# Kernel optimization log

Measured on AMD Instinct MI355X. Metric: run time of the kernel, lower is better.

Reference implementation:

```python
import jax, jax.numpy as jnp
import numpy as np

EPS = 1e-3  # Keras LayerNormalization default epsilon


def layernorm(x, g, b):
    mu = jnp.mean(x, axis=-1, keepdims=True)
    var = jnp.var(x, axis=-1, keepdims=True)
    return (x - mu) * jax.lax.rsqrt(var + EPS) * g + b


def setup_inputs() -> dict:
    key = jax.random.key(0)
    ks = jax.random.split(key, 16)
    B, T, C = 2, 2048, 1024
    F = 4 * C
    std = 0.02
    inp = {
        "x": jax.random.normal(ks[0], (B, T, C), jnp.float32),
        "ln1_g": jnp.ones((C,), jnp.float32),
        "ln1_b": jnp.zeros((C,), jnp.float32),
        "Wq": std * jax.random.normal(ks[1], (C, C), jnp.float32),
        "bq": jnp.zeros((C,), jnp.float32),
        "Wk": std * jax.random.normal(ks[2], (C, C), jnp.float32),
        "bk": jnp.zeros((C,), jnp.float32),
        "Wv": std * jax.random.normal(ks[3], (C, C), jnp.float32),
        "bv": jnp.zeros((C,), jnp.float32),
        "ln2_g": jnp.ones((C,), jnp.float32),
        "ln2_b": jnp.zeros((C,), jnp.float32),
        "W1": std * jax.random.normal(ks[4], (C, F), jnp.float32),
        "b1": jnp.zeros((F,), jnp.float32),
        "W2": std * jax.random.normal(ks[5], (F, C), jnp.float32),
        "b2": jnp.zeros((C,), jnp.float32),
    }
    return inp


N_HEADS = 16


def reference(x, ln1_g, ln1_b, Wq, bq, Wk, bk, Wv, bv, ln2_g, ln2_b, W1, b1, W2, b2):
    B, T, C = x.shape
    H = N_HEADS
    D = C // H

    h = layernorm(x, ln1_g, ln1_b)
    # [B,T,C] -> [B,H,T,D]
    def split_heads(y):
        return y.reshape(B, T, H, D).transpose(0, 2, 1, 3)

    q = split_heads(h @ Wq + bq)
    k = split_heads(h @ Wk + bk)
    v = split_heads(h @ Wv + bv)

    # Faithful to original: scores = K @ Q^T, i.e. scores[i,j] = k_i . q_j
    scores = jnp.einsum("bhid,bhjd->bhij", k, q) / jnp.sqrt(jnp.float32(D))
    causal = jnp.tril(jnp.ones((T, T), bool))  # [T,T]
    scores = jnp.where(causal[None, None], scores, -jnp.inf)
    w = jax.nn.softmax(scores, axis=-1)
    attn = jnp.einsum("bhij,bhjd->bhid", w, v)  # [B,H,T,D]
    attn = attn.transpose(0, 2, 1, 3).reshape(B, T, C)
    x = x + attn

    h2 = layernorm(x, ln2_g, ln2_b)
    ffn = jax.nn.gelu(h2 @ W1 + b1, approximate=False) @ W2 + b2
    x = x + ffn
    return x
```

## Files before the change

kernel.cpp:

```cpp
#include <hip/hip_runtime.h>
#include <hip/hip_bf16.h>
#include <math.h>

typedef __hip_bfloat16 bf16;
typedef __attribute__((ext_vector_type(8))) short bf16x8;
typedef __attribute__((ext_vector_type(4))) float f32x4;

__device__ __forceinline__ unsigned short f2bf_rne(float f) {
  unsigned u = __float_as_uint(f);
  u += 0x7fffu + ((u >> 16) & 1u);
  return (unsigned short)(u >> 16);
}
__device__ __forceinline__ float bf2f(unsigned short s) {
  return __uint_as_float(((unsigned)s) << 16);
}

__device__ __forceinline__ float gelu_fast(float v) {
  float u = v * (0.7978845608f + 0.0356774081f * v * v);
  float t = __builtin_amdgcn_exp2f(u * 2.8853900818f);
  float r = __builtin_amdgcn_rcpf(t + 1.0f);
  return v - v * r;
}

#define GLOBAL_AS __attribute__((address_space(1)))
#define LDS_AS __attribute__((address_space(3)))
__device__ __forceinline__ void gl2lds16(const void* g, void* l) {
  __builtin_amdgcn_global_load_lds((const GLOBAL_AS void*)g, (LDS_AS void*)l, 16, 0, 0);
}

__device__ __forceinline__ int swz8(int f, int nwg) {
  return (f & 7) * (nwg >> 3) + (f >> 3);
}

__device__ __forceinline__ void ln_body(const float* __restrict__ x,
                                        const float* __restrict__ g,
                                        const float* __restrict__ b,
                                        bf16* __restrict__ h, int row, int t) {
  const float4 xv = ((const float4*)(x + (size_t)row * 1024))[t];
  float s = xv.x + xv.y + xv.z + xv.w;
  float sq = xv.x * xv.x + xv.y * xv.y + xv.z * xv.z + xv.w * xv.w;
  #pragma unroll
  for (int m = 1; m < 64; m <<= 1) { s += __shfl_xor(s, m); sq += __shfl_xor(sq, m); }
  __shared__ float ps[4], pq[4];
  if ((t & 63) == 0) { ps[t >> 6] = s; pq[t >> 6] = sq; }
  __syncthreads();
  s = ps[0] + ps[1] + ps[2] + ps[3];
  sq = pq[0] + pq[1] + pq[2] + pq[3];
  float mean = s * (1.0f / 1024.0f);
  float var = sq * (1.0f / 1024.0f) - mean * mean;
  float rs = rsqrtf(var + 1e-3f);
  float4 gv = ((const float4*)g)[t];
  float4 bv = ((const float4*)b)[t];
  ushort4 o;
  o.x = f2bf_rne((xv.x - mean) * rs * gv.x + bv.x);
  o.y = f2bf_rne((xv.y - mean) * rs * gv.y + bv.y);
  o.z = f2bf_rne((xv.z - mean) * rs * gv.z + bv.z);
  o.w = f2bf_rne((xv.w - mean) * rs * gv.w + bv.w);
  ((ushort4*)(h + (size_t)row * 1024))[t] = o;
}

__global__ __launch_bounds__(256) void ln_kernel(const float* __restrict__ x,
                                                 const float* __restrict__ g,
                                                 const float* __restrict__ b,
                                                 bf16* __restrict__ h) {
  ln_body(x, g, b, h, blockIdx.x, threadIdx.x);
}

__device__ __forceinline__ void tr_tile(const float* __restrict__ W, bf16* __restrict__ WT,
                                        int R, int Cc, int bx, int by, int t) {
  __shared__ float tile[32][33];
  int tx = t & 31, ty = t >> 5;
  #pragma unroll
  for (int k = 0; k < 4; k++) {
    int rr = ty + k * 8;
    tile[rr][tx] = W[(size_t)(by + rr) * Cc + bx + tx];
  }
  __syncthreads();
  unsigned short* out = reinterpret_cast<unsigned short*>(WT);
  #pragma unroll
  for (int k = 0; k < 4; k++) {
    int rr = ty + k * 8;
    out[(size_t)(bx + rr) * R + by + tx] = f2bf_rne(tile[tx][rr]);
  }
}

__global__ __launch_bounds__(256) void prep_fused(const float* __restrict__ x,
                                                  const float* __restrict__ ln1g,
                                                  const float* __restrict__ ln1b,
                                                  bf16* __restrict__ h,
                                                  const float* __restrict__ Wq,
                                                  const float* __restrict__ Wk,
                                                  const float* __restrict__ Wv,
                                                  const float* __restrict__ W1,
                                                  const float* __restrict__ W2,
                                                  bf16* __restrict__ WqkT,
                                                  bf16* __restrict__ W1T,
                                                  bf16* __restrict__ W2T) {
  int id = blockIdx.x, t = threadIdx.x;
  if (id < 4096) { ln_body(x, ln1g, ln1b, h, id, t); return; }
  id -= 4096;
  if (id < 3072) {
    int sect = id >> 10, r = id & 1023;
    const float* W = sect == 0 ? Wq : (sect == 1 ? Wk : Wv);
    bf16* WT = WqkT + (size_t)sect * 1048576;
    tr_tile(W, WT, 1024, 1024, (r & 31) * 32, (r >> 5) * 32, t);
  } else if (id < 7168) {
    int r = id - 3072;
    tr_tile(W1, W1T, 1024, 4096, (r & 127) * 32, (r >> 7) * 32, t);
  } else {
    int r = id - 7168;
    tr_tile(W2, W2T, 4096, 1024, (r & 31) * 32, (r >> 5) * 32, t);
  }
}

__device__ __forceinline__ void mainloop_256(const bf16* __restrict__ A,
                                             const bf16* __restrict__ BT,
                                             int lda, int nk, int m0, int n0,
                                             char* ldsb, int t,
                                             f32x4 (&acc)[8][4]) {
  const int lane = t & 63, wave = t >> 6;
  const int l = lane & 15, quad = lane >> 4;
  const int wm = (wave >> 2) * 128, wn = (wave & 3) * 64;
  const int srow = wave * 8 + (lane >> 3);
  const int scol = ((lane & 7) ^ (lane >> 3)) * 8;
  const int grp0 = (quad ^ (l & 7)) * 16;
  const int grp1 = ((4 + quad) ^ (l & 7)) * 16;

  bf16x8 a[4][2], b01[2][2], b23[2][2];

  auto stA = [&](int buf, int half, int kt) {
    const bf16* s = A + (size_t)(m0 + half * 128 + srow) * lda + kt * 64 + scol;
    char* d = ldsb + buf * 65536 + half * 16384 + wave * 1024;
    gl2lds16(s, d);
    gl2lds16(s + (size_t)64 * lda, d + 8192);
  };
  auto stB = [&](int buf, int half, int kt) {
    const bf16* s = BT + (size_t)(n0 + half * 128 + srow) * lda + kt * 64 + scol;
    char* d = ldsb + buf * 65536 + 32768 + half * 16384 + wave * 1024;
    gl2lds16(s, d);
    gl2lds16(s + (size_t)64 * lda, d + 8192);
  };
  auto rdA = [&](int buf, int mh) {
    const char* base = ldsb + buf * 65536 + (wm + mh * 64 + l) * 128;
    #pragma unroll
    for (int ii = 0; ii < 4; ii++) {
      a[ii][0] = *(const bf16x8*)(base + ii * 2048 + grp0);
      a[ii][1] = *(const bf16x8*)(base + ii * 2048 + grp1);
    }
  };
  auto rdB = [&](int buf, int nh, bf16x8 (&bb)[2][2]) {
    const char* base = ldsb + buf * 65536 + 32768 + (wn + nh * 32 + l) * 128;
    #pragma unroll
    for (int jj = 0; jj < 2; jj++) {
      bb[jj][0] = *(const bf16x8*)(base + jj * 2048 + grp0);
      bb[jj][1] = *(const bf16x8*)(base + jj * 2048 + grp1);
    }
  };
  auto mm4 = [&](int mi, bf16x8 (&bb)[2][2], int nj) {
    #pragma unroll
    for (int ii = 0; ii < 4; ii++)
      #pragma unroll
      for (int jj = 0; jj < 2; jj++) {
        acc[mi + ii][nj + jj] = __builtin_amdgcn_mfma_f32_16x16x32_bf16(
            a[ii][0], bb[jj][0], acc[mi + ii][nj + jj], 0, 0, 0);
        acc[mi + ii][nj + jj] = __builtin_amdgcn_mfma_f32_16x16x32_bf16(
            a[ii][1], bb[jj][1], acc[mi + ii][nj + jj], 0, 0, 0);
      }
  };

#define BARX() __builtin_amdgcn_s_barrier()
#define LGKM0() do { asm volatile("s_waitcnt lgkmcnt(0)" ::: "memory"); \
                     __builtin_amdgcn_sched_barrier(0); } while (0)
#define HALF4(BC, DOA, SAB, SAK, DOB, SBB, SBK, VMN)                      \
  do {                                                                    \
    rdA(BC, 0); rdB(BC, 0, b01);                                          \
    if (DOA) stA(SAB, 0, SAK);                                            \
    BARX(); LGKM0();                                                      \
    __builtin_amdgcn_s_setprio(1); mm4(0, b01, 0);                        \
    __builtin_amdgcn_s_setprio(0); BARX();                                \
    rdB(BC, 1, b23);                                                      \
    if (DOA) stA(SAB, 1, SAK);                                            \
    BARX(); LGKM0();                                                      \
    __builtin_amdgcn_s_setprio(1); mm4(0, b23, 2);                        \
    __builtin_amdgcn_s_setprio(0); BARX();                                \
    rdA(BC, 1);                                                           \
    if (DOB) stB(SBB, 0, SBK);                                            \
    BARX(); LGKM0();                                                      \
    __builtin_amdgcn_s_setprio(1); mm4(4, b01, 0);                        \
    __builtin_amdgcn_s_setprio(0); BARX();                                \
    if (DOB) stB(SBB, 1, SBK);                                            \
    BARX();                                                               \
    __builtin_amdgcn_s_setprio(1); mm4(4, b23, 2);                        \
    __builtin_amdgcn_s_setprio(0);                                        \
    asm volatile("s_waitcnt vmcnt(" VMN ")" ::: "memory");                \
    BARX();                                                               \
  } while (0)

  const int nt = nk >> 6;
  stA(0, 0, 0); stA(0, 1, 0);
  stB(0, 0, 0); stB(0, 1, 0);
  stB(1, 0, 1); stB(1, 1, 1);
  asm volatile("s_waitcnt vmcnt(4)" ::: "memory");
  BARX();
  int tt = 0;
  for (; tt + 2 < nt; tt += 2) {
    HALF4(0, 1, 1, tt + 1, 1, 0, tt + 2, "4");
    HALF4(1, 1, 0, tt + 2, 1, 1, tt + 3, "4");
  }
  HALF4(0, 1, 1, tt + 1, 0, 0, 0, "0");
  HALF4(1, 0, 0, 0, 0, 0, 0, "0");
#undef HALF4
#undef LGKM0
#undef BARX
}

__global__ __launch_bounds__(512, 2) void gemm_ffn1(const bf16* __restrict__ A,
                                                    const bf16* __restrict__ BT,
                                                    const float* __restrict__ bias,
                                                    bf16* __restrict__ out,
                                                    int N, int K) {
  extern __shared__ char lds[];
  int t = threadIdx.x;
  int nf = swz8(blockIdx.x, gridDim.x);
  int n0 = (nf & 15) * 256, m0 = (nf >> 4) * 256;
  f32x4 acc[8][4];
  #pragma unroll
  for (int i = 0; i < 8; i++)
    #pragma unroll
    for (int j = 0; j < 4; j++) acc[i][j] = (f32x4){0.f, 0.f, 0.f, 0.f};
  mainloop_256(A, BT, K, K, m0, n0, lds, t, acc);

  int lane = t & 63, wave = t >> 6;
  int l = lane & 15, quad = lane >> 4;
  int wm = (wave >> 2) * 128, wn = (wave & 3) * 64;
  int r4 = quad * 4;
  unsigned short* os = reinterpret_cast<unsigned short*>(out);
  #pragma unroll
  for (int i = 0; i < 8; i++)
    #pragma unroll
    for (int j = 0; j < 4; j++) {
      int col = n0 + wn + j * 16 + l;
      float bval = bias[col];
      #pragma unroll
      for (int r = 0; r < 4; r++) {
        int row = m0 + wm + i * 16 + r4 + r;
        os[(size_t)row * N + col] = f2bf_rne(gelu_fast(acc[i][j][r] + bval));
      }
    }
}

__global__ __launch_bounds__(512, 2) void gemm_ffn2(const bf16* __restrict__ A,
                                                    const bf16* __restrict__ BT,
                                                    unsigned short* __restrict__ p0,
                                                    unsigned short* __restrict__ p1,
                                                    unsigned short* __restrict__ p2,
                                                    unsigned short* __restrict__ p3) {
  extern __shared__ char lds[];
  int t = threadIdx.x;
  int nf = swz8(blockIdx.x, gridDim.x);
  int n0 = (nf & 3) * 256, m0 = ((nf >> 2) & 15) * 256;
  int z = nf >> 6;
  f32x4 acc[8][4];
  #pragma unroll
  for (int i = 0; i < 8; i++)
    #pragma unroll
    for (int j = 0; j < 4; j++) acc[i][j] = (f32x4){0.f, 0.f, 0.f, 0.f};
  mainloop_256(A + z * 1024, BT + z * 1024, 4096, 1024, m0, n0, lds, t, acc);

  unsigned short* p = z == 0 ? p0 : (z == 1 ? p1 : (z == 2 ? p2 : p3));
  int lane = t & 63, wave = t >> 6;
  int l = lane & 15, quad = lane >> 4;
  int wm = (wave >> 2) * 128, wn = (wave & 3) * 64;
  int r4 = quad * 4;
  #pragma unroll
  for (int i = 0; i < 8; i++)
    #pragma unroll
    for (int j = 0; j < 4; j++) {
      int col = n0 + wn + j * 16 + l;
      #pragma unroll
      for (int r = 0; r < 4; r++) {
        int row = m0 + wm + i * 16 + r4 + r;
        p[(size_t)row * 1024 + col] = f2bf_rne(acc[i][j][r]);
      }
    }
}

__global__ __launch_bounds__(256) void reduce_ffn2(const unsigned short* __restrict__ p0,
                                                   const unsigned short* __restrict__ p1,
                                                   const unsigned short* __restrict__ p2,
                                                   const unsigned short* __restrict__ p3,
                                                   const float* __restrict__ x1,
                                                   const float* __restrict__ bias,
                                                   float* __restrict__ out) {
  int row = blockIdx.x, t = threadIdx.x;
  size_t base = (size_t)row * 1024;
  ushort4 a = ((const ushort4*)(p0 + base))[t];
  ushort4 b = ((const ushort4*)(p1 + base))[t];
  ushort4 c = ((const ushort4*)(p2 + base))[t];
  ushort4 d = ((const ushort4*)(p3 + base))[t];
  float4 xv = ((const float4*)(x1 + base))[t];
  float4 bv = ((const float4*)bias)[t];
  float4 o;
  o.x = (bf2f(a.x) + bf2f(b.x)) + (bf2f(c.x) + bf2f(d.x)) + xv.x + bv.x;
  o.y = (bf2f(a.y) + bf2f(b.y)) + (bf2f(c.y) + bf2f(d.y)) + xv.y + bv.y;
  o.z = (bf2f(a.z) + bf2f(b.z)) + (bf2f(c.z) + bf2f(d.z)) + xv.z + bv.z;
  o.w = (bf2f(a.w) + bf2f(b.w)) + (bf2f(c.w) + bf2f(d.w)) + xv.w + bv.w;
  ((float4*)(out + base))[t] = o;
}

__global__ __launch_bounds__(512, 2) void gemm_qkv(const bf16* __restrict__ A,
                                                   const bf16* __restrict__ BT,
                                                   const float* __restrict__ bq,
                                                   const float* __restrict__ bk,
                                                   const float* __restrict__ bv,
                                                   bf16* __restrict__ qb,
                                                   bf16* __restrict__ kb,
                                                   bf16* __restrict__ vt,
                                                   int K) {
  extern __shared__ char lds[];
  int t = threadIdx.x;
  int nf = swz8(blockIdx.x, gridDim.x);
  int n0 = (nf % 12) * 256, m0 = (nf / 12) * 256;
  f32x4 acc[8][4];
  #pragma unroll
  for (int i = 0; i < 8; i++)
    #pragma unroll
    for (int j = 0; j < 4; j++) acc[i][j] = (f32x4){0.f, 0.f, 0.f, 0.f};
  mainloop_256(A, BT, K, K, m0, n0, lds, t, acc);

  int lane = t & 63, wave = t >> 6;
  int l = lane & 15, quad = lane >> 4;
  int wm = (wave >> 2) * 128, wn = (wave & 3) * 64;
  int sect = n0 >> 10;
  const float* bias = sect == 0 ? bq : (sect == 1 ? bk : bv);
  int r4 = quad * 4;
  #pragma unroll
  for (int i = 0; i < 8; i++)
    #pragma unroll
    for (int j = 0; j < 4; j++) {
      int col = n0 + wn + j * 16 + l;
      int c1 = col & 1023;
      float bval = bias[c1];
      int row0 = m0 + wm + i * 16 + r4;
      if (sect < 2) {
        bf16* o = sect == 0 ? qb : kb;
        unsigned short* os = reinterpret_cast<unsigned short*>(o);
        #pragma unroll
        for (int r = 0; r < 4; r++)
          os[(size_t)(row0 + r) * 1024 + c1] = f2bf_rne(acc[i][j][r] + bval);
      } else {
        int hh = c1 >> 6, d = c1 & 63;
        int b = row0 >> 11, t0 = row0 & 2047;
        ushort4 pk;
        pk.x = f2bf_rne(acc[i][j][0] + bval);
        pk.y = f2bf_rne(acc[i][j][1] + bval);
        pk.z = f2bf_rne(acc[i][j][2] + bval);
        pk.w = f2bf_rne(acc[i][j][3] + bval);
        *(ushort4*)((unsigned short*)vt + (size_t)((b * 16 + hh) * 64 + d) * 2048 + t0) = pk;
      }
    }
}

__global__ __launch_bounds__(512, 4) void attn_mfma(const bf16* __restrict__ qb,
                                                    const bf16* __restrict__ kb,
                                                    const bf16* __restrict__ vt,
                                                    const float* __restrict__ x,
                                                    float* __restrict__ x1) {
  extern __shared__ char alds[];
  char* KVb = alds;
  char* Pb  = alds + 65536;
  int t = threadIdx.x;
  int bh = blockIdx.x;
  int b = bh >> 4, h = bh & 15;
  size_t qk_base = (size_t)b * 2048 * 1024 + (size_t)h * 64;
  size_t vt_base = (size_t)bh * 64 * 2048;
  int lane = t & 63, wave = t >> 6;
  int g = wave >> 2, w4 = wave & 3;
  int l = lane & 15, quad = lane >> 4;
  int sw = l & 7;
  int srow8 = lane >> 3;
  int scol = ((lane & 7) ^ srow8) * 8;
  const float cs = 0.125f * 1.44269504088896f;
  int it = 31 - blockIdx.y;
  int i0 = it * 64;
  int njt = it + 1;
  int iblk = i0 + w4 * 16;

  if (g == 0) {
    #pragma unroll
    for (int c = 0; c < 2; c++) {
      int rr = w4 * 16 + c * 8 + srow8;
      gl2lds16(kb + qk_base + (size_t)(i0 + rr) * 1024 + scol,
               Pb + w4 * 2048 + c * 1024);
      gl2lds16(qb + qk_base + (size_t)rr * 1024 + scol,
               KVb + w4 * 2048 + c * 1024);
      gl2lds16(vt + vt_base + (size_t)rr * 2048 + scol,
               KVb + 8192 + w4 * 2048 + c * 1024);
    }
  } else if (njt > 1) {
    #pragma unroll
    for (int c = 0; c < 2; c++) {
      int rr = w4 * 16 + c * 8 + srow8;
      gl2lds16(qb + qk_base + (size_t)(64 + rr) * 1024 + scol,
               KVb + 32768 + w4 * 2048 + c * 1024);
      gl2lds16(vt + vt_base + (size_t)rr * 2048 + 64 + scol,
               KVb + 32768 + 8192 + w4 * 2048 + c * 1024);
    }
  }
  __syncthreads();

  const char* qr = Pb + w4 * 2048 + l * 128;
  bf16x8 qf0 = *(const bf16x8*)(qr + ((quad ^ sw) * 16));
  bf16x8 qf1 = *(const bf16x8*)(qr + (((4 + quad) ^ sw) * 16));
  __syncthreads();

  float lsum = 0.f;
  f32x4 Oacc[4];
  #pragma unroll
  for (int dt = 0; dt < 4; dt++) Oacc[dt] = (f32x4){0.f, 0.f, 0.f, 0.f};

  char* Pw = Pb + wave * 2048 + l * 128;
  char* KVg = KVb + g * 32768;
  int nstep = (njt + 1) >> 1;
  int buf = 0;
  for (int s = 0; s < nstep; s++) {
    int jt = 2 * s + g;
    if (jt + 2 < njt) {
      int j1 = (jt + 2) * 64;
      #pragma unroll
      for (int c = 0; c < 2; c++) {
        int rr = w4 * 16 + c * 8 + srow8;
        gl2lds16(qb + qk_base + (size_t)(j1 + rr) * 1024 + scol,
                 KVg + (buf ^ 1) * 16384 + w4 * 2048 + c * 1024);
        gl2lds16(vt + vt_base + (size_t)rr * 2048 + j1 + scol,
                 KVg + (buf ^ 1) * 16384 + 8192 + w4 * 2048 + c * 1024);
      }
    }
    if (jt < njt) {
      int j0v = jt * 64;
      const bf16* Kb = (const bf16*)(KVg + buf * 16384);
      #pragma unroll
      for (int nt = 0; nt < 4; nt++) {
        int jb = j0v + nt * 16;
        uint2 pk;
        if (jb > iblk + 15) {
          pk.x = 0u; pk.y = 0u;
        } else {
          const bf16* kr = Kb + (nt * 16 + l) * 64;
          bf16x8 kf0 = *(const bf16x8*)(kr + ((quad ^ sw) * 8));
          bf16x8 kf1 = *(const bf16x8*)(kr + (((4 + quad) ^ sw) * 8));
          f32x4 sv = (f32x4){0.f, 0.f, 0.f, 0.f};
          __builtin_amdgcn_s_setprio(1);
          sv = __builtin_amdgcn_mfma_f32_16x16x32_bf16(kf0, qf0, sv, 0, 0, 0);
          sv = __builtin_amdgcn_mfma_f32_16x16x32_bf16(kf1, qf1, sv, 0, 0, 0);
          __builtin_amdgcn_s_setprio(0);
          float p0, p1, p2, p3;
          if (jb + 15 <= iblk) {
            p0 = __builtin_amdgcn_exp2f(sv[0] * cs);
            p1 = __builtin_amdgcn_exp2f(sv[1] * cs);
            p2 = __builtin_amdgcn_exp2f(sv[2] * cs);
            p3 = __builtin_amdgcn_exp2f(sv[3] * cs);
          } else {
            int i_ = iblk + l, jbase = jb + quad * 4;
            p0 = (jbase + 0 > i_) ? 0.f : __builtin_amdgcn_exp2f(sv[0] * cs);
            p1 = (jbase + 1 > i_) ? 0.f : __builtin_amdgcn_exp2f(sv[1] * cs);
            p2 = (jbase + 2 > i_) ? 0.f : __builtin_amdgcn_exp2f(sv[2] * cs);
            p3 = (jbase + 3 > i_) ? 0.f : __builtin_amdgcn_exp2f(sv[3] * cs);
          }
          lsum += (p0 + p1) + (p2 + p3);
          union { __hip_bfloat162 h2; unsigned u; } c0u, c1u;
          c0u.h2 = __float22bfloat162_rn(make_float2(p0, p1));
          c1u.h2 = __float22bfloat162_rn(make_float2(p2, p3));
          pk.x = c0u.u; pk.y = c1u.u;
        }
        *(uint2*)(Pw + (((nt * 2 + (quad >> 1)) ^ sw) << 4) + ((quad & 1) << 3)) = pk;
      }
      asm volatile("s_waitcnt lgkmcnt(0)" ::: "memory");

      bf16x8 ap0 = *(const bf16x8*)(Pw + ((quad ^ sw) << 4));
      bf16x8 ap1 = *(const bf16x8*)(Pw + (((4 + quad) ^ sw) << 4));
      const bf16* Vb = (const bf16*)(KVg + buf * 16384 + 8192);
      __builtin_amdgcn_s_setprio(1);
      #pragma unroll
      for (int dt = 0; dt < 4; dt++) {
        const bf16* vr = Vb + (dt * 16 + l) * 64;
        bf16x8 bv0 = *(const bf16x8*)(vr + ((quad ^ sw) * 8));
        bf16x8 bv1 = *(const bf16x8*)(vr + (((4 + quad) ^ sw) * 8));
        Oacc[dt] = __builtin_amdgcn_mfma_f32_16x16x32_bf16(ap0, bv0, Oacc[dt], 0, 0, 0);
        Oacc[dt] = __builtin_amdgcn_mfma_f32_16x16x32_bf16(ap1, bv1, Oacc[dt], 0, 0, 0);
      }
      __builtin_amdgcn_s_setprio(0);
    }
    __syncthreads();
    buf ^= 1;
  }

  float* F = (float*)KVb;
  int fbase = w4 * 1088;
  if (g == 1) {
    #pragma unroll
    for (int dt = 0; dt < 4; dt++)
      #pragma unroll
      for (int r = 0; r < 4; r++)
        F[fbase + (dt * 4 + r) * 64 + lane] = Oacc[dt][r];
    F[fbase + 1024 + lane] = lsum;
  }
  __syncthreads();
  if (g == 0) {
    #pragma unroll
    for (int dt = 0; dt < 4; dt++)
      #pragma unroll
      for (int r = 0; r < 4; r++)
        Oacc[dt][r] += F[fbase + (dt * 4 + r) * 64 + lane];
    lsum += F[fbase + 1024 + lane];
    lsum += __shfl_xor(lsum, 16);
    lsum += __shfl_xor(lsum, 32);
    #pragma unroll
    for (int r = 0; r < 4; r++) {
      float lv = __shfl(lsum, quad * 4 + r);
      float inv = 1.0f / lv;
      int row = iblk + quad * 4 + r;
      size_t gi = qk_base + (size_t)row * 1024;
      #pragma unroll
      for (int dt = 0; dt < 4; dt++) {
        int d = dt * 16 + l;
        x1[gi + d] = x[gi + d] + Oacc[dt][r] * inv;
      }
    }
  }
}

extern "C" void kernel_launch(void* const* d_in, const int* in_sizes, int n_in,
                              void* d_out, int out_size, void* d_ws, size_t ws_size,
                              hipStream_t stream) {
  const float* x    = (const float*)d_in[0];
  const float* ln1g = (const float*)d_in[1];
  const float* ln1b = (const float*)d_in[2];
  const float* Wq   = (const float*)d_in[3];
  const float* bq   = (const float*)d_in[4];
  const float* Wk   = (const float*)d_in[5];
  const float* bk   = (const float*)d_in[6];
  const float* Wv   = (const float*)d_in[7];
  const float* bv   = (const float*)d_in[8];
  const float* ln2g = (const float*)d_in[9];
  const float* ln2b = (const float*)d_in[10];
  const float* W1   = (const float*)d_in[11];
  const float* b1   = (const float*)d_in[12];
  const float* W2   = (const float*)d_in[13];
  const float* b2   = (const float*)d_in[14];

  char* ws = (char*)d_ws;
  float* x1  = (float*)(ws + 0);
  bf16* h    = (bf16*)(ws + 16777216);
  bf16* WqkT = (bf16*)(ws + 25165824);
  bf16* W1T  = (bf16*)(ws + 31457280);
  bf16* W2T  = (bf16*)(ws + 39845888);
  bf16* qb   = (bf16*)(ws + 48234496);
  bf16* kb   = (bf16*)(ws + 56623104);
  bf16* vt   = (bf16*)(ws + 65011712);
  bf16* act  = (bf16*)(ws + 73400320);

  static bool s_attr_done = false;
  if (!s_attr_done) {
    hipFuncSetAttribute(reinterpret_cast<const void*>(gemm_qkv),
                        hipFuncAttributeMaxDynamicSharedMemorySize, 131072);
    hipFuncSetAttribute(reinterpret_cast<const void*>(gemm_ffn1),
                        hipFuncAttributeMaxDynamicSharedMemorySize, 131072);
    hipFuncSetAttribute(reinterpret_cast<const void*>(gemm_ffn2),
                        hipFuncAttributeMaxDynamicSharedMemorySize, 131072);
    hipFuncSetAttribute(reinterpret_cast<const void*>(attn_mfma),
                        hipFuncAttributeMaxDynamicSharedMemorySize, 81920);
    s_attr_done = true;
  }

  prep_fused<<<15360, 256, 0, stream>>>(x, ln1g, ln1b, h,
                                        Wq, Wk, Wv, W1, W2, WqkT, W1T, W2T);
  gemm_qkv<<<192, 512, 131072, stream>>>(h, WqkT, bq, bk, bv, qb, kb, vt, 1024);
  attn_mfma<<<dim3(32, 32), 512, 81920, stream>>>(qb, kb, vt, x, x1);
  ln_kernel<<<4096, 256, 0, stream>>>(x1, ln2g, ln2b, h);
  gemm_ffn1<<<256, 512, 131072, stream>>>(h, W1T, b1, act, 4096, 1024);
  gemm_ffn2<<<256, 512, 131072, stream>>>(act, W2T,
      (unsigned short*)qb, (unsigned short*)kb, (unsigned short*)vt, (unsigned short*)h);
  reduce_ffn2<<<4096, 256, 0, stream>>>((const unsigned short*)qb, (const unsigned short*)kb,
                                        (const unsigned short*)vt, (const unsigned short*)h,
                                        x1, b2, (float*)d_out);
}
```

Baseline: 291.6 us.

## Fuse LN2 into attention and split-K reduce into FFN2 via atomic counters

Removes the standalone LayerNorm-2 kernel: the last attention block to finish for each row group, detected with an atomic counter, computes LN2 for those rows. Removes the standalone split-K reduction by having FFN2 blocks spin-wait on a per-tile counter until all four K-slices are written, then each block reduces a quarter of the tile. Also drops the s_setprio hints in the attention MFMA loops. This saves two launches and some memory traffic, but adds spin-waiting that can deadlock if the co-dependent blocks are not co-resident, and it serializes the LN2 work onto a few blocks.

```diff
diff --git a/kernel.cpp b/kernel.cpp
--- a/kernel.cpp
+++ b/kernel.cpp
@@ -59,13 +59,6 @@
   ((ushort4*)(h + (size_t)row * 1024))[t] = o;
 }
 
-__global__ __launch_bounds__(256) void ln_kernel(const float* __restrict__ x,
-                                                 const float* __restrict__ g,
-                                                 const float* __restrict__ b,
-                                                 bf16* __restrict__ h) {
-  ln_body(x, g, b, h, blockIdx.x, threadIdx.x);
-}
-
 __device__ __forceinline__ void tr_tile(const float* __restrict__ W, bf16* __restrict__ WT,
                                         int R, int Cc, int bx, int by, int t) {
   __shared__ float tile[32][33];
@@ -95,8 +88,10 @@
                                                   const float* __restrict__ W2,
                                                   bf16* __restrict__ WqkT,
                                                   bf16* __restrict__ W1T,
-                                                  bf16* __restrict__ W2T) {
+                                                  bf16* __restrict__ W2T,
+                                                  int* __restrict__ cnt) {
   int id = blockIdx.x, t = threadIdx.x;
+  if (id == 0 && t < 128) cnt[t] = 0;
   if (id < 4096) { ln_body(x, ln1g, ln1b, h, id, t); return; }
   id -= 4096;
   if (id < 3072) {
@@ -254,12 +249,17 @@
                                                     unsigned short* __restrict__ p0,
                                                     unsigned short* __restrict__ p1,
                                                     unsigned short* __restrict__ p2,
-                                                    unsigned short* __restrict__ p3) {
+                                                    unsigned short* __restrict__ p3,
+                                                    const float* __restrict__ x1,
+                                                    const float* __restrict__ bias,
+                                                    float* __restrict__ out,
+                                                    int* __restrict__ cnt) {
   extern __shared__ char lds[];
   int t = threadIdx.x;
   int nf = swz8(blockIdx.x, gridDim.x);
   int n0 = (nf & 3) * 256, m0 = ((nf >> 2) & 15) * 256;
   int z = nf >> 6;
+  int tid = (m0 >> 8) * 4 + (n0 >> 8);
   f32x4 acc[8][4];
   #pragma unroll
   for (int i = 0; i < 8; i++)
@@ -283,29 +283,35 @@
         p[(size_t)row * 1024 + col] = f2bf_rne(acc[i][j][r]);
       }
     }
-}
-
-__global__ __launch_bounds__(256) void reduce_ffn2(const unsigned short* __restrict__ p0,
-                                                   const unsigned short* __restrict__ p1,
-                                                   const unsigned short* __restrict__ p2,
-                                                   const unsigned short* __restrict__ p3,
-                                                   const float* __restrict__ x1,
-                                                   const float* __restrict__ bias,
-                                                   float* __restrict__ out) {
-  int row = blockIdx.x, t = threadIdx.x;
-  size_t base = (size_t)row * 1024;
-  ushort4 a = ((const ushort4*)(p0 + base))[t];
-  ushort4 b = ((const ushort4*)(p1 + base))[t];
-  ushort4 c = ((const ushort4*)(p2 + base))[t];
-  ushort4 d = ((const ushort4*)(p3 + base))[t];
-  float4 xv = ((const float4*)(x1 + base))[t];
-  float4 bv = ((const float4*)bias)[t];
-  float4 o;
-  o.x = (bf2f(a.x) + bf2f(b.x)) + (bf2f(c.x) + bf2f(d.x)) + xv.x + bv.x;
-  o.y = (bf2f(a.y) + bf2f(b.y)) + (bf2f(c.y) + bf2f(d.y)) + xv.y + bv.y;
-  o.z = (bf2f(a.z) + bf2f(b.z)) + (bf2f(c.z) + bf2f(d.z)) + xv.z + bv.z;
-  o.w = (bf2f(a.w) + bf2f(b.w)) + (bf2f(c.w) + bf2f(d.w)) + xv.w + bv.w;
-  ((float4*)(out + base))[t] = o;
+
+  __threadfence();
+  __syncthreads();
+  if (t == 0) {
+    atomicAdd(cnt + tid, 1);
+    while (atomicAdd(cnt + tid, 0) < 4) __builtin_amdgcn_s_sleep(2);
+  }
+  __syncthreads();
+  __threadfence();
+  {
+    int col4 = t & 63;
+    float4 bv = ((const float4*)bias)[(n0 >> 2) + col4];
+    int rbase = m0 + z * 64 + (t >> 6) * 8;
+    #pragma unroll
+    for (int k = 0; k < 8; k++) {
+      size_t base = (size_t)(rbase + k) * 1024 + n0;
+      ushort4 a = ((const ushort4*)(p0 + base))[col4];
+      ushort4 b = ((const ushort4*)(p1 + base))[col4];
+      ushort4 c = ((const ushort4*)(p2 + base))[col4];
+      ushort4 d = ((const ushort4*)(p3 + base))[col4];
+      float4 xv = ((const float4*)(x1 + base))[col4];
+      float4 o;
+      o.x = (bf2f(a.x) + bf2f(b.x)) + (bf2f(c.x) + bf2f(d.x)) + xv.x + bv.x;
+      o.y = (bf2f(a.y) + bf2f(b.y)) + (bf2f(c.y) + bf2f(d.y)) + xv.y + bv.y;
+      o.z = (bf2f(a.z) + bf2f(b.z)) + (bf2f(c.z) + bf2f(d.z)) + xv.z + bv.z;
+      o.w = (bf2f(a.w) + bf2f(b.w)) + (bf2f(c.w) + bf2f(d.w)) + xv.w + bv.w;
+      ((float4*)(out + base))[col4] = o;
+    }
+  }
 }
 
 __global__ __launch_bounds__(512, 2) void gemm_qkv(const bf16* __restrict__ A,
@@ -365,7 +371,11 @@
                                                     const bf16* __restrict__ kb,
                                                     const bf16* __restrict__ vt,
                                                     const float* __restrict__ x,
-                                                    float* __restrict__ x1) {
+                                                    float* __restrict__ x1,
+                                                    const float* __restrict__ ln2g,
+                                                    const float* __restrict__ ln2b,
+                                                    bf16* __restrict__ hout,
+                                                    int* __restrict__ cnt) {
   extern __shared__ char alds[];
   char* KVb = alds;
   char* Pb  = alds + 65536;
@@ -450,10 +460,8 @@
           bf16x8 kf0 = *(const bf16x8*)(kr + ((quad ^ sw) * 8));
           bf16x8 kf1 = *(const bf16x8*)(kr + (((4 + quad) ^ sw) * 8));
           f32x4 sv = (f32x4){0.f, 0.f, 0.f, 0.f};
-          __builtin_amdgcn_s_setprio(1);
           sv = __builtin_amdgcn_mfma_f32_16x16x32_bf16(kf0, qf0, sv, 0, 0, 0);
           sv = __builtin_amdgcn_mfma_f32_16x16x32_bf16(kf1, qf1, sv, 0, 0, 0);
-          __builtin_amdgcn_s_setprio(0);
           float p0, p1, p2, p3;
           if (jb + 15 <= iblk) {
             p0 = __builtin_amdgcn_exp2f(sv[0] * cs);
@@ -480,7 +488,6 @@
       bf16x8 ap0 = *(const bf16x8*)(Pw + ((quad ^ sw) << 4));
       bf16x8 ap1 = *(const bf16x8*)(Pw + (((4 + quad) ^ sw) << 4));
       const bf16* Vb = (const bf16*)(KVg + buf * 16384 + 8192);
-      __builtin_amdgcn_s_setprio(1);
       #pragma unroll
       for (int dt = 0; dt < 4; dt++) {
         const bf16* vr = Vb + (dt * 16 + l) * 64;
@@ -489,7 +496,6 @@
         Oacc[dt] = __builtin_amdgcn_mfma_f32_16x16x32_bf16(ap0, bv0, Oacc[dt], 0, 0, 0);
         Oacc[dt] = __builtin_amdgcn_mfma_f32_16x16x32_bf16(ap1, bv1, Oacc[dt], 0, 0, 0);
       }
-      __builtin_amdgcn_s_setprio(0);
     }
     __syncthreads();
     buf ^= 1;
@@ -525,6 +531,47 @@
       for (int dt = 0; dt < 4; dt++) {
         int d = dt * 16 + l;
         x1[gi + d] = x[gi + d] + Oacc[dt][r] * inv;
+      }
+    }
+  }
+
+  __threadfence();
+  __syncthreads();
+  int* scnt = (int*)(alds + 18432);
+  if (t == 0) *scnt = atomicAdd(cnt + (b * 32 + (int)blockIdx.y), 1);
+  __syncthreads();
+  if (*scnt == 15) {
+    __threadfence();
+    int rowbase = b * 2048 + i0 + wave * 8;
+    const float4* gv4 = (const float4*)ln2g;
+    const float4* bv4 = (const float4*)ln2b;
+    for (int rr = 0; rr < 8; rr++) {
+      int row = rowbase + rr;
+      const float4* xr = (const float4*)(x1 + (size_t)row * 1024);
+      float4 v[4];
+      float s = 0.f, sq = 0.f;
+      #pragma unroll
+      for (int p = 0; p < 4; p++) {
+        v[p] = xr[p * 64 + lane];
+        s += (v[p].x + v[p].y) + (v[p].z + v[p].w);
+        sq += (v[p].x * v[p].x + v[p].y * v[p].y) + (v[p].z * v[p].z + v[p].w * v[p].w);
+      }
+      #pragma unroll
+      for (int m = 1; m < 64; m <<= 1) { s += __shfl_xor(s, m); sq += __shfl_xor(sq, m); }
+      float mean = s * (1.0f / 1024.0f);
+      float var = sq * (1.0f / 1024.0f) - mean * mean;
+      float rs = rsqrtf(var + 1e-3f);
+      ushort4* hr = (ushort4*)(hout + (size_t)row * 1024);
+      #pragma unroll
+      for (int p = 0; p < 4; p++) {
+        float4 gv = gv4[p * 64 + lane];
+        float4 bv = bv4[p * 64 + lane];
+        ushort4 o;
+        o.x = f2bf_rne((v[p].x - mean) * rs * gv.x + bv.x);
+        o.y = f2bf_rne((v[p].y - mean) * rs * gv.y + bv.y);
+        o.z = f2bf_rne((v[p].z - mean) * rs * gv.z + bv.z);
+        o.w = f2bf_rne((v[p].w - mean) * rs * gv.w + bv.w);
+        hr[p * 64 + lane] = o;
       }
     }
   }
@@ -559,6 +606,7 @@
   bf16* kb   = (bf16*)(ws + 56623104);
   bf16* vt   = (bf16*)(ws + 65011712);
   bf16* act  = (bf16*)(ws + 73400320);
+  int*  cnt  = (int*)(ws + 106954752);
 
   static bool s_attr_done = false;
   if (!s_attr_done) {
@@ -574,14 +622,12 @@
   }
 
   prep_fused<<<15360, 256, 0, stream>>>(x, ln1g, ln1b, h,
-                                        Wq, Wk, Wv, W1, W2, WqkT, W1T, W2T);
+                                        Wq, Wk, Wv, W1, W2, WqkT, W1T, W2T, cnt);
   gemm_qkv<<<192, 512, 131072, stream>>>(h, WqkT, bq, bk, bv, qb, kb, vt, 1024);
-  attn_mfma<<<dim3(32, 32), 512, 81920, stream>>>(qb, kb, vt, x, x1);
-  ln_kernel<<<4096, 256, 0, stream>>>(x1, ln2g, ln2b, h);
+  attn_mfma<<<dim3(32, 32), 512, 81920, stream>>>(qb, kb, vt, x, x1,
+                                                  ln2g, ln2b, h, cnt);
   gemm_ffn1<<<256, 512, 131072, stream>>>(h, W1T, b1, act, 4096, 1024);
   gemm_ffn2<<<256, 512, 131072, stream>>>(act, W2T,
-      (unsigned short*)qb, (unsigned short*)kb, (unsigned short*)vt, (unsigned short*)h);
-  reduce_ffn2<<<4096, 256, 0, stream>>>((const unsigned short*)qb, (const unsigned short*)kb,
-                                        (const unsigned short*)vt, (const unsigned short*)h,
-                                        x1, b2, (float*)d_out);
-}
+      (unsigned short*)qb, (unsigned short*)kb, (unsigned short*)vt, (unsigned short*)h,
+      x1, b2, (float*)d_out, cnt + 64);
+}
```

Result: slower. 695.2 us (+138.4%).
